# Kernel tuning notes

Measured on AMD Instinct MI355X. Metric: run time of the kernel, lower is better.

## Reference

```python
import jax, jax.numpy as jnp
import numpy as np

N = 50000          # num nodes
E = 800000         # num edges (avg degree 16)
D_IN = 128         # input_size
H = 128            # hidden_size
BN_EPS = 1e-5


def setup_inputs() -> dict:
    key = jax.random.key(0)
    ks = jax.random.split(key, 16)
    std = 1.0 / np.sqrt(H)
    u = lambda k, shape: jax.random.uniform(k, shape, jnp.float32, -std, std)
    return {
        "x": jax.random.normal(ks[0], (N, D_IN), jnp.float32),
        "hx": jax.random.normal(ks[1], (N, H), jnp.float32),
        "cx": jax.random.normal(ks[2], (N, H), jnp.float32),
        "edge_src": jax.random.randint(ks[3], (E,), 0, N, jnp.int32),
        "edge_dst": jax.random.randint(ks[4], (E,), 0, N, jnp.int32),
        "edge_weight": jax.random.uniform(ks[5], (E,), jnp.float32) / 16.0,  # ~normalized adj values
        "gcn_weight": u(ks[6], (D_IN, H)),
        "bias": u(ks[7], (H,)),
        "x2h_w": u(ks[8], (4 * H, H)),
        "x2h_b": u(ks[9], (4 * H,)),
        "h2h_w": u(ks[10], (4 * H, H)),
        "h2h_b": u(ks[11], (4 * H,)),
        "bn_gamma": u(ks[12], (H,)),
        "bn_beta": u(ks[13], (H,)),
        "bn_mean": jnp.zeros((H,), jnp.float32),
        "bn_var": jnp.ones((H,), jnp.float32),
    }


def reference(x, hx, cx, edge_src, edge_dst, edge_weight, gcn_weight, bias,
              x2h_w, x2h_b, h2h_w, h2h_b, bn_gamma, bn_beta, bn_mean, bn_var):
    # GCN: support = x @ W, then sparse adj @ support via gather/segment-sum
    support = x @ gcn_weight                                   # (N, H)
    msgs = edge_weight[:, None] * support[edge_src]            # (E, H)
    agg = jax.ops.segment_sum(msgs, edge_dst, num_segments=N)  # (N, H) = spmm(adj, support)
    h = jax.nn.relu(agg)
    # dropout: eval mode -> identity
    h = h + bias
    # BatchNorm1d (eval mode, running stats)
    h = (h - bn_mean) * jax.lax.rsqrt(bn_var + BN_EPS) * bn_gamma + bn_beta
    # fused LSTM gates: x2h(h) + h2h(hx)
    gates = h @ x2h_w.T + x2h_b + hx @ h2h_w.T + h2h_b         # (N, 4H)
    i_g, f_g, g_g, o_g = jnp.split(gates, 4, axis=1)
    cy = cx * jax.nn.sigmoid(f_g) + jax.nn.sigmoid(i_g) * jnp.tanh(g_g)
    hy = jax.nn.sigmoid(o_g) * jnp.tanh(cy)
    return hy, cy
```

## Files before the change

kernel.cpp:

```cpp
#include <hip/hip_runtime.h>

#define NN 50000
#define NE 800000
#define HH 128
#define BN_EPS 1e-5f
#define SCAN_NB ((NN + 255) / 256)

typedef unsigned short u16;
typedef unsigned int u32;
typedef short bf16x8 __attribute__((ext_vector_type(8)));
typedef float f32x4 __attribute__((ext_vector_type(4)));

static __device__ __forceinline__ float bf2f(u16 u){
  union { u32 i; float f; } v; v.i = ((u32)u) << 16; return v.f;
}
static __device__ __forceinline__ u16 f2bf(float f){
  union { float f; u32 i; } v; v.f = f;
  u32 x = v.i;
  return (u16)((x + 0x7fffu + ((x >> 16) & 1u)) >> 16);
}
static __device__ __forceinline__ float sigm(float x){
  return 1.f / (1.f + __expf(-x));
}
static __device__ __forceinline__ float tanh_fast(float x){
  return 1.f - 2.f / (1.f + __expf(2.f * x));
}


__global__ void hist_kernel(const int* __restrict__ dst, int* __restrict__ counts, int E){
  int e = blockIdx.x * blockDim.x + threadIdx.x;
  if (e < E) atomicAdd(&counts[dst[e]], 1);
}


__global__ __launch_bounds__(256) void scan_bsum(
    const int* __restrict__ counts, int* __restrict__ bsums, int n){
  int i = blockIdx.x * 256 + threadIdx.x;
  int v = (i < n) ? counts[i] : 0;
#pragma unroll
  for (int off = 1; off < 64; off <<= 1) v += __shfl_xor(v, off);
  __shared__ int ws[4];
  if ((threadIdx.x & 63) == 0) ws[threadIdx.x >> 6] = v;
  __syncthreads();
  if (threadIdx.x == 0) bsums[blockIdx.x] = ws[0] + ws[1] + ws[2] + ws[3];
}

__global__ __launch_bounds__(256) void scan_tops(int* __restrict__ bsums, int nb){
  __shared__ int sh[256];
  int t = threadIdx.x;
  int v = (t < nb) ? bsums[t] : 0;
  sh[t] = v;
  __syncthreads();
  for (int off = 1; off < 256; off <<= 1){
    int u = (t >= off) ? sh[t - off] : 0;
    __syncthreads();
    sh[t] += u;
    __syncthreads();
  }
  if (t < nb) bsums[t] = sh[t] - v;
}

__global__ __launch_bounds__(256) void scan_final(
    const int* __restrict__ counts, const int* __restrict__ bsums,
    int* __restrict__ offs, int* __restrict__ cursor, int n){
  __shared__ int sh[256];
  int t = threadIdx.x;
  int i = blockIdx.x * 256 + t;
  int v = (i < n) ? counts[i] : 0;
  sh[t] = v;
  __syncthreads();
  for (int off = 1; off < 256; off <<= 1){
    int u = (t >= off) ? sh[t - off] : 0;
    __syncthreads();
    sh[t] += u;
    __syncthreads();
  }
  int excl = sh[t] - v + bsums[blockIdx.x];
  if (i < n){ offs[i] = excl; cursor[i] = excl; }
}

__global__ void scatter_kernel(const int* __restrict__ src, const int* __restrict__ dst,
                               const float* __restrict__ w, int* __restrict__ cursor,
                               int2* __restrict__ esw, int E){
  int e = blockIdx.x * blockDim.x + threadIdx.x;
  if (e < E){
    int d = dst[e];
    int pos = atomicAdd(&cursor[d], 1);
    esw[pos] = make_int2(src[e], __float_as_int(w[e]));
  }
}

__global__ void prep_pack(const float* __restrict__ x2hw, const float* __restrict__ h2hw,
                          const float* __restrict__ x2hb, const float* __restrict__ h2hb,
                          const float* __restrict__ gcnw,
                          u16* __restrict__ wcat, u16* __restrict__ wgcn,
                          float* __restrict__ bsum, int* __restrict__ counts){
  int i = blockIdx.x * blockDim.x + threadIdx.x;
  int n = i >> 8, k = i & 255;
  float v = (k < 128) ? x2hw[n * 128 + k] : h2hw[n * 128 + (k - 128)];
  int nt = n >> 4, lc = n & 15;
  int kk = k >> 5, lq = (k >> 3) & 3, e = k & 7;
  wcat[(((nt * 8 + kk) * 64) + lq * 16 + lc) * 8 + e] = f2bf(v);
  if (i < 16384){
    int nn = i >> 7, kx = i & 127;
    wgcn[i] = f2bf(gcnw[kx * 128 + nn]);
  }
  if (i < 512) bsum[i] = x2hb[i] + h2hb[i];
  if (i < NN) counts[i] = 0;
}

__global__ __launch_bounds__(256) void support_mfma(
    const float* __restrict__ x, const u16* __restrict__ wgcn,
    u16* __restrict__ support, int N){
  int tid = threadIdx.x;
  int wave = tid >> 6, lane = tid & 63;
  int c = lane & 15, q = lane >> 4;
  int row0 = blockIdx.x * 64 + wave * 16;
  int arow = row0 + c; if (arow > N - 1) arow = N - 1;
  f32x4 acc[8];
#pragma unroll
  for (int t = 0; t < 8; t++) acc[t] = (f32x4){0.f, 0.f, 0.f, 0.f};

  const u16* wp = wgcn + (size_t)c * 128 + q * 8;
#pragma unroll
  for (int k0 = 0; k0 < 128; k0 += 32){
    const float* ap = x + (size_t)arow * 128 + k0 + q * 8;
    float4 f0 = *(const float4*)ap;
    float4 f1 = *(const float4*)(ap + 4);
    u16 tmp[8] = {f2bf(f0.x), f2bf(f0.y), f2bf(f0.z), f2bf(f0.w),
                  f2bf(f1.x), f2bf(f1.y), f2bf(f1.z), f2bf(f1.w)};
    bf16x8 afrag = *(bf16x8*)tmp;
#pragma unroll
    for (int t = 0; t < 8; t++){
      bf16x8 bfrag = *(const bf16x8*)(wp + (size_t)t * 16 * 128 + k0);
      acc[t] = __builtin_amdgcn_mfma_f32_16x16x32_bf16(afrag, bfrag, acc[t], 0, 0, 0);
    }
  }
#pragma unroll
  for (int t = 0; t < 8; t++){
#pragma unroll
    for (int j = 0; j < 4; j++){
      int r = row0 + q * 4 + j;
      if (r < N) support[(size_t)r * 128 + t * 16 + c] = f2bf(acc[t][j]);
    }
  }
}

__global__ __launch_bounds__(256) void agg_bn3(
    const u16* __restrict__ support, const int2* __restrict__ esw,
    const int* __restrict__ offs, const int* __restrict__ counts,
    const float* __restrict__ bias, const float* __restrict__ gamma,
    const float* __restrict__ beta, const float* __restrict__ mean,
    const float* __restrict__ var, const float* __restrict__ hx,
    u16* __restrict__ hbn, u16* __restrict__ hxb, int N){
  int wid = blockIdx.x * 4 + (threadIdx.x >> 6);
  int lane = threadIdx.x & 63;
  if (wid >= N) return;
  int c = lane * 2;
  float2 hv = *(const float2*)(hx + (size_t)wid * HH + c);
  int start = offs[wid];
  int deg   = counts[wid];
  float a0 = 0.f, a1 = 0.f;
  int e = 0;
  for (; e + 8 <= deg; e += 8){
    int2 ev[8]; u32 u[8];
#pragma unroll
    for (int k = 0; k < 8; k++) ev[k] = esw[start + e + k];
#pragma unroll
    for (int k = 0; k < 8; k++)
      u[k] = *(const u32*)(support + (size_t)ev[k].x * HH + c);
#pragma unroll
    for (int k = 0; k < 8; k++){
      float g = __int_as_float(ev[k].y);
      a0 = fmaf(g, bf2f((u16)(u[k] & 0xffffu)), a0);
      a1 = fmaf(g, bf2f((u16)(u[k] >> 16)), a1);
    }
  }
  for (; e + 4 <= deg; e += 4){
    int2 ev[4]; u32 u[4];
#pragma unroll
    for (int k = 0; k < 4; k++) ev[k] = esw[start + e + k];
#pragma unroll
    for (int k = 0; k < 4; k++)
      u[k] = *(const u32*)(support + (size_t)ev[k].x * HH + c);
#pragma unroll
    for (int k = 0; k < 4; k++){
      float g = __int_as_float(ev[k].y);
      a0 = fmaf(g, bf2f((u16)(u[k] & 0xffffu)), a0);
      a1 = fmaf(g, bf2f((u16)(u[k] >> 16)), a1);
    }
  }
  for (; e < deg; e++){
    int2 ev = esw[start + e];
    float g = __int_as_float(ev.y);
    u32 ui = *(const u32*)(support + (size_t)ev.x * HH + c);
    a0 = fmaf(g, bf2f((u16)(ui & 0xffffu)), a0);
    a1 = fmaf(g, bf2f((u16)(ui >> 16)), a1);
  }
  float h0 = fmaxf(a0, 0.f) + bias[c];
  float h1 = fmaxf(a1, 0.f) + bias[c + 1];
  float s0 = gamma[c]     * rsqrtf(var[c]     + BN_EPS);
  float s1 = gamma[c + 1] * rsqrtf(var[c + 1] + BN_EPS);
  float r0 = (h0 - mean[c])     * s0 + beta[c];
  float r1 = (h1 - mean[c + 1]) * s1 + beta[c + 1];
  u32 pack = (u32)f2bf(r0) | ((u32)f2bf(r1) << 16);
  *(u32*)(hbn + (size_t)wid * HH + c) = pack;
  u32 hp = (u32)f2bf(hv.x) | ((u32)f2bf(hv.y) << 16);
  *(u32*)(hxb + (size_t)wid * HH + c) = hp;
}

__global__ __launch_bounds__(1024, 1) void gates_mfma6(
    const u16* __restrict__ hbn, const u16* __restrict__ hxb,
    const u16* __restrict__ wcat, const float* __restrict__ bsum,
    const float* __restrict__ cx, float* __restrict__ out, int N){
  __shared__ float lbuf[2][8][16][64];
  int tid = threadIdx.x;
  int wave = tid >> 6, lane = tid & 63;
  int c = lane & 15, q = lane >> 4;
  int cw = wave & 7, kh = wave >> 3;
  int hloc = cw * 16 + c;

  const bf16x8* wsrc = (const bf16x8*)wcat;
  bf16x8 btile[4][4];
#pragma unroll
  for (int g = 0; g < 4; g++)
#pragma unroll
    for (int kk = 0; kk < 4; kk++)
      btile[g][kk] = wsrc[((size_t)((g * 8 + cw) * 8) + kh * 4 + kk) * 64 + lane];

  float bi = 0.f, bf_ = 0.f, bg = 0.f, bo = 0.f;
  if (kh == 0){
    bi  = bsum[hloc];
    bf_ = bsum[128 + hloc];
    bg  = bsum[256 + hloc];
    bo  = bsum[384 + hloc];
  }
  const u16* abuf = kh ? hxb : hbn;
  const size_t NH = (size_t)N * HH;
  const int nchunk = N >> 4;
  int p = 0;
  int chunk = blockIdx.x;

  bf16x8 a_cur[4];
  if (chunk < nchunk){
    const u16* ap = abuf + (size_t)((chunk << 4) + c) * 128 + q * 8;
#pragma unroll
    for (int kk = 0; kk < 4; kk++) a_cur[kk] = *(const bf16x8*)(ap + kk * 32);
  }

  for (; chunk < nchunk; chunk += gridDim.x){
    int row0 = chunk << 4;
    int nxt = chunk + gridDim.x;
    int prow = (nxt < nchunk) ? (nxt << 4) : 0;
    const u16* pnp = abuf + (size_t)(prow + c) * 128 + q * 8;
    bf16x8 a_nxt[4];
#pragma unroll
    for (int kk = 0; kk < 4; kk++) a_nxt[kk] = *(const bf16x8*)(pnp + kk * 32);
    float cxv[4];
    if (kh == 0){
#pragma unroll
      for (int j = 0; j < 4; j++)
        cxv[j] = cx[(size_t)(row0 + q * 4 + j) * HH + hloc];
    }

    f32x4 acc[4];
#pragma unroll
    for (int g = 0; g < 4; g++) acc[g] = (f32x4){0.f, 0.f, 0.f, 0.f};
#pragma unroll
    for (int kk = 0; kk < 4; kk++){
#pragma unroll
      for (int g = 0; g < 4; g++)
        acc[g] = __builtin_amdgcn_mfma_f32_16x16x32_bf16(a_cur[kk], btile[g][kk], acc[g], 0, 0, 0);
    }
    if (kh == 1){
#pragma unroll
      for (int g = 0; g < 4; g++)
#pragma unroll
        for (int j = 0; j < 4; j++)
          lbuf[p][cw][g * 4 + j][lane] = acc[g][j];
    }
    __syncthreads();
    if (kh == 0){
#pragma unroll
      for (int j = 0; j < 4; j++){
        int r = row0 + q * 4 + j;
        float gi = acc[0][j] + lbuf[p][cw][0 + j][lane]  + bi;
        float gf = acc[1][j] + lbuf[p][cw][4 + j][lane]  + bf_;
        float gg = acc[2][j] + lbuf[p][cw][8 + j][lane]  + bg;
        float go = acc[3][j] + lbuf[p][cw][12 + j][lane] + bo;
        float is = sigm(gi), fs = sigm(gf), gt = tanh_fast(gg), os = sigm(go);
        float cyv = cxv[j] * fs + is * gt;
        out[(size_t)r * HH + hloc]      = os * tanh_fast(cyv);
        out[NH + (size_t)r * HH + hloc] = cyv;
      }
    }
#pragma unroll
    for (int kk = 0; kk < 4; kk++) a_cur[kk] = a_nxt[kk];
    p ^= 1;
  }
}


extern "C" void kernel_launch(void* const* d_in, const int* in_sizes, int n_in,
                              void* d_out, int out_size, void* d_ws, size_t ws_size,
                              hipStream_t stream){
  const float* x     = (const float*)d_in[0];
  const float* hx    = (const float*)d_in[1];
  const float* cx    = (const float*)d_in[2];
  const int*   esrc  = (const int*)d_in[3];
  const int*   edst  = (const int*)d_in[4];
  const float* ew    = (const float*)d_in[5];
  const float* gcn_w = (const float*)d_in[6];
  const float* bias  = (const float*)d_in[7];
  const float* x2hw  = (const float*)d_in[8];
  const float* x2hb  = (const float*)d_in[9];
  const float* h2hw  = (const float*)d_in[10];
  const float* h2hb  = (const float*)d_in[11];
  const float* bn_g  = (const float*)d_in[12];
  const float* bn_b  = (const float*)d_in[13];
  const float* bn_m  = (const float*)d_in[14];
  const float* bn_v  = (const float*)d_in[15];
  float* out = (float*)d_out;

  char* w = (char*)d_ws;
  u16* support = (u16*)w; w += (((size_t)NN * HH * 2) + 255) & ~(size_t)255;
  u16* hbn     = (u16*)w; w += (((size_t)NN * HH * 2) + 255) & ~(size_t)255;
  u16* hxb     = (u16*)w; w += (((size_t)NN * HH * 2) + 255) & ~(size_t)255;
  int* counts  = (int*)w; w += (((size_t)NN * 4) + 255) & ~(size_t)255;
  int* offs    = (int*)w; w += (((size_t)NN * 4) + 255) & ~(size_t)255;
  int* cursor  = (int*)w; w += (((size_t)NN * 4) + 255) & ~(size_t)255;
  int* bsums   = (int*)w; w += (((size_t)SCAN_NB * 4) + 255) & ~(size_t)255;
  int2* esw    = (int2*)w; w += (((size_t)NE * 8) + 255) & ~(size_t)255;
  u16* wcat    = (u16*)w; w += (((size_t)512 * 256 * 2) + 255) & ~(size_t)255;
  u16* wgcn    = (u16*)w; w += (((size_t)128 * 128 * 2) + 255) & ~(size_t)255;
  float* bsum  = (float*)w; w += (((size_t)512 * 4) + 255) & ~(size_t)255;

  prep_pack<<<512, 256, 0, stream>>>(x2hw, h2hw, x2hb, h2hb, gcn_w, wcat, wgcn, bsum, counts);
  hist_kernel<<<(NE + 255) / 256, 256, 0, stream>>>(edst, counts, NE);
  scan_bsum<<<SCAN_NB, 256, 0, stream>>>(counts, bsums, NN);
  scan_tops<<<1, 256, 0, stream>>>(bsums, SCAN_NB);
  scan_final<<<SCAN_NB, 256, 0, stream>>>(counts, bsums, offs, cursor, NN);
  scatter_kernel<<<(NE + 255) / 256, 256, 0, stream>>>(esrc, edst, ew, cursor, esw, NE);
  support_mfma<<<(NN + 63) / 64, 256, 0, stream>>>(x, wgcn, support, NN);
  agg_bn3<<<(NN + 3) / 4, 256, 0, stream>>>(support, esw, offs, counts,
                                            bias, bn_g, bn_b, bn_m, bn_v, hx, hbn, hxb, NN);
  gates_mfma6<<<512, 1024, 0, stream>>>(hbn, hxb, wcat, bsum, cx, out, NN);
}
```

Baseline: 360.6 us.

## Fuse prep/hist and scatter/support launches, merge scan stages, split gates over columns

Merges independent kernels into combined launches: weight packing runs alongside the degree histogram, and edge scatter runs alongside the support GEMM. The block-sum scan is folded into the final scan, so every block rescans the block sums itself. The counts array is now cleared with a memset. The gates kernel is split across two column halves with 512-thread blocks and a 2D grid, aiming to cut launch overhead and raise occupancy at the cost of more redundant A-tile loads.

```diff
diff --git a/kernel.cpp b/kernel.cpp
--- a/kernel.cpp
+++ b/kernel.cpp
@@ -5,6 +5,10 @@
 #define HH 128
 #define BN_EPS 1e-5f
 #define SCAN_NB ((NN + 255) / 256)
+#define PREP_NB 512
+#define HIST_NB ((NE + 255) / 256)
+#define SCAT_NB ((NE + 255) / 256)
+#define SUPP_NB ((NN + 63) / 64)
 
 typedef unsigned short u16;
 typedef unsigned int u32;
@@ -26,10 +30,29 @@
   return 1.f - 2.f / (1.f + __expf(2.f * x));
 }
 
-
-__global__ void hist_kernel(const int* __restrict__ dst, int* __restrict__ counts, int E){
-  int e = blockIdx.x * blockDim.x + threadIdx.x;
-  if (e < E) atomicAdd(&counts[dst[e]], 1);
+__global__ __launch_bounds__(256) void fused_prep_hist(
+    const float* __restrict__ x2hw, const float* __restrict__ h2hw,
+    const float* __restrict__ x2hb, const float* __restrict__ h2hb,
+    const float* __restrict__ gcnw,
+    u16* __restrict__ wcat, u16* __restrict__ wgcn, float* __restrict__ bsum,
+    const int* __restrict__ edst, int* __restrict__ counts){
+  int bid = blockIdx.x;
+  if (bid < PREP_NB){
+    int i = bid * 256 + threadIdx.x;
+    int n = i >> 8, k = i & 255;
+    float v = (k < 128) ? x2hw[n * 128 + k] : h2hw[n * 128 + (k - 128)];
+    int nt = n >> 4, lc = n & 15;
+    int kk = k >> 5, lq = (k >> 3) & 3, e = k & 7;
+    wcat[(((nt * 8 + kk) * 64) + lq * 16 + lc) * 8 + e] = f2bf(v);
+    if (i < 16384){
+      int nn = i >> 7, kx = i & 127;
+      wgcn[i] = f2bf(gcnw[kx * 128 + nn]);
+    }
+    if (i < 512) bsum[i] = x2hb[i] + h2hb[i];
+  } else {
+    int e = (bid - PREP_NB) * 256 + threadIdx.x;
+    if (e < NE) atomicAdd(&counts[edst[e]], 1);
+  }
 }
 
 
@@ -45,26 +68,21 @@
   if (threadIdx.x == 0) bsums[blockIdx.x] = ws[0] + ws[1] + ws[2] + ws[3];
 }
 
-__global__ __launch_bounds__(256) void scan_tops(int* __restrict__ bsums, int nb){
-  __shared__ int sh[256];
+__global__ __launch_bounds__(256) void scan_final2(
+    const int* __restrict__ counts, const int* __restrict__ bsums,
+    int* __restrict__ offs, int* __restrict__ cursor, int n, int nb){
+  __shared__ int sh[256], bs[256];
   int t = threadIdx.x;
-  int v = (t < nb) ? bsums[t] : 0;
-  sh[t] = v;
+  int bv = (t < nb) ? bsums[t] : 0;
+  bs[t] = bv;
   __syncthreads();
   for (int off = 1; off < 256; off <<= 1){
-    int u = (t >= off) ? sh[t - off] : 0;
-    __syncthreads();
-    sh[t] += u;
-    __syncthreads();
-  }
-  if (t < nb) bsums[t] = sh[t] - v;
-}
-
-__global__ __launch_bounds__(256) void scan_final(
-    const int* __restrict__ counts, const int* __restrict__ bsums,
-    int* __restrict__ offs, int* __restrict__ cursor, int n){
-  __shared__ int sh[256];
-  int t = threadIdx.x;
+    int u = (t >= off) ? bs[t - off] : 0;
+    __syncthreads();
+    bs[t] += u;
+    __syncthreads();
+  }
+  int bexcl = (blockIdx.x > 0) ? bs[blockIdx.x - 1] : 0;
   int i = blockIdx.x * 256 + t;
   int v = (i < n) ? counts[i] : 0;
   sh[t] = v;
@@ -75,47 +93,30 @@
     sh[t] += u;
     __syncthreads();
   }
-  int excl = sh[t] - v + bsums[blockIdx.x];
+  int excl = sh[t] - v + bexcl;
   if (i < n){ offs[i] = excl; cursor[i] = excl; }
 }
 
-__global__ void scatter_kernel(const int* __restrict__ src, const int* __restrict__ dst,
-                               const float* __restrict__ w, int* __restrict__ cursor,
-                               int2* __restrict__ esw, int E){
-  int e = blockIdx.x * blockDim.x + threadIdx.x;
-  if (e < E){
-    int d = dst[e];
-    int pos = atomicAdd(&cursor[d], 1);
-    esw[pos] = make_int2(src[e], __float_as_int(w[e]));
-  }
-}
-
-__global__ void prep_pack(const float* __restrict__ x2hw, const float* __restrict__ h2hw,
-                          const float* __restrict__ x2hb, const float* __restrict__ h2hb,
-                          const float* __restrict__ gcnw,
-                          u16* __restrict__ wcat, u16* __restrict__ wgcn,
-                          float* __restrict__ bsum, int* __restrict__ counts){
-  int i = blockIdx.x * blockDim.x + threadIdx.x;
-  int n = i >> 8, k = i & 255;
-  float v = (k < 128) ? x2hw[n * 128 + k] : h2hw[n * 128 + (k - 128)];
-  int nt = n >> 4, lc = n & 15;
-  int kk = k >> 5, lq = (k >> 3) & 3, e = k & 7;
-  wcat[(((nt * 8 + kk) * 64) + lq * 16 + lc) * 8 + e] = f2bf(v);
-  if (i < 16384){
-    int nn = i >> 7, kx = i & 127;
-    wgcn[i] = f2bf(gcnw[kx * 128 + nn]);
-  }
-  if (i < 512) bsum[i] = x2hb[i] + h2hb[i];
-  if (i < NN) counts[i] = 0;
-}
-
-__global__ __launch_bounds__(256) void support_mfma(
+__global__ __launch_bounds__(256) void fused_scatter_support(
+    const int* __restrict__ src, const int* __restrict__ dst,
+    const float* __restrict__ w, int* __restrict__ cursor, int2* __restrict__ esw,
     const float* __restrict__ x, const u16* __restrict__ wgcn,
     u16* __restrict__ support, int N){
+  int bid = blockIdx.x;
+  if (bid < SCAT_NB){
+    int e = bid * 256 + threadIdx.x;
+    if (e < NE){
+      int d = dst[e];
+      int pos = atomicAdd(&cursor[d], 1);
+      esw[pos] = make_int2(src[e], __float_as_int(w[e]));
+    }
+    return;
+  }
+  int sbid = bid - SCAT_NB;
   int tid = threadIdx.x;
   int wave = tid >> 6, lane = tid & 63;
   int c = lane & 15, q = lane >> 4;
-  int row0 = blockIdx.x * 64 + wave * 16;
+  int row0 = sbid * 64 + wave * 16;
   int arow = row0 + c; if (arow > N - 1) arow = N - 1;
   f32x4 acc[8];
 #pragma unroll
@@ -209,16 +210,17 @@
   *(u32*)(hxb + (size_t)wid * HH + c) = hp;
 }
 
-__global__ __launch_bounds__(1024, 1) void gates_mfma6(
+__global__ __launch_bounds__(512, 4) void gates_mfma7(
     const u16* __restrict__ hbn, const u16* __restrict__ hxb,
     const u16* __restrict__ wcat, const float* __restrict__ bsum,
     const float* __restrict__ cx, float* __restrict__ out, int N){
-  __shared__ float lbuf[2][8][16][64];
+  __shared__ float lbuf[2][4][16][64];
   int tid = threadIdx.x;
   int wave = tid >> 6, lane = tid & 63;
   int c = lane & 15, q = lane >> 4;
-  int cw = wave & 7, kh = wave >> 3;
-  int hloc = cw * 16 + c;
+  int cw = wave & 3, kh = wave >> 2;
+  int hh = blockIdx.y;
+  int hloc = hh * 64 + cw * 16 + c;
 
   const bf16x8* wsrc = (const bf16x8*)wcat;
   bf16x8 btile[4][4];
@@ -226,7 +228,7 @@
   for (int g = 0; g < 4; g++)
 #pragma unroll
     for (int kk = 0; kk < 4; kk++)
-      btile[g][kk] = wsrc[((size_t)((g * 8 + cw) * 8) + kh * 4 + kk) * 64 + lane];
+      btile[g][kk] = wsrc[((size_t)((g * 8 + hh * 4 + cw) * 8) + kh * 4 + kk) * 64 + lane];
 
   float bi = 0.f, bf_ = 0.f, bg = 0.f, bo = 0.f;
   if (kh == 0){
@@ -335,14 +337,14 @@
   u16* wgcn    = (u16*)w; w += (((size_t)128 * 128 * 2) + 255) & ~(size_t)255;
   float* bsum  = (float*)w; w += (((size_t)512 * 4) + 255) & ~(size_t)255;
 
-  prep_pack<<<512, 256, 0, stream>>>(x2hw, h2hw, x2hb, h2hb, gcn_w, wcat, wgcn, bsum, counts);
-  hist_kernel<<<(NE + 255) / 256, 256, 0, stream>>>(edst, counts, NE);
+  hipMemsetAsync(counts, 0, (size_t)NN * 4, stream);
+  fused_prep_hist<<<PREP_NB + HIST_NB, 256, 0, stream>>>(
+      x2hw, h2hw, x2hb, h2hb, gcn_w, wcat, wgcn, bsum, edst, counts);
   scan_bsum<<<SCAN_NB, 256, 0, stream>>>(counts, bsums, NN);
-  scan_tops<<<1, 256, 0, stream>>>(bsums, SCAN_NB);
-  scan_final<<<SCAN_NB, 256, 0, stream>>>(counts, bsums, offs, cursor, NN);
-  scatter_kernel<<<(NE + 255) / 256, 256, 0, stream>>>(esrc, edst, ew, cursor, esw, NE);
-  support_mfma<<<(NN + 63) / 64, 256, 0, stream>>>(x, wgcn, support, NN);
+  scan_final2<<<SCAN_NB, 256, 0, stream>>>(counts, bsums, offs, cursor, NN, SCAN_NB);
+  fused_scatter_support<<<SCAT_NB + SUPP_NB, 256, 0, stream>>>(
+      esrc, edst, ew, cursor, esw, x, wgcn, support, NN);
   agg_bn3<<<(NN + 3) / 4, 256, 0, stream>>>(support, esw, offs, counts,
                                             bias, bn_g, bn_b, bn_m, bn_v, hx, hbn, hxb, NN);
-  gates_mfma6<<<512, 1024, 0, stream>>>(hbn, hxb, wcat, bsum, cx, out, NN);
-}
+  gates_mfma7<<<dim3(256, 2), 512, 0, stream>>>(hbn, hxb, wcat, bsum, cx, out, NN);
+}
```

Measured after the change: 349.5 us. 1.03x faster.
